# Performance work log

Hardware: AMD Instinct MI355X
Metric: run time of the kernel (lower is better)

The kernel has to match this reference:

```python
import jax, jax.numpy as jnp
import numpy as np

B, S, HID = 2, 2048, 4096
NH, NKV = 32, 8
HD = HID // NH          # 128
G = NH // NKV           # 4 groups per kv head
ROPE_THETA = 10000.0


def setup_inputs() -> dict:
    key = jax.random.key(0)
    ks = jax.random.split(key, 5)
    scale = 0.02
    return {
        "hidden_states": jax.random.normal(ks[0], (B, S, HID), dtype=jnp.float32),
        "Wq": jax.random.normal(ks[1], (NH * HD, HID), dtype=jnp.float32) * scale,
        "Wk": jax.random.normal(ks[2], (NKV * HD, HID), dtype=jnp.float32) * scale,
        "Wv": jax.random.normal(ks[3], (NKV * HD, HID), dtype=jnp.float32) * scale,
        "Wo": jax.random.normal(ks[4], (HID, HID), dtype=jnp.float32) * scale,
    }


def _rope_cos_sin(seq_len, head_dim, dtype):
    inv_freq = 1.0 / (ROPE_THETA ** (jnp.arange(0, head_dim, 2, dtype=jnp.float32) / head_dim))
    pos = jnp.arange(seq_len, dtype=jnp.float32)
    freqs = pos[:, None] * inv_freq[None, :]          # [S, HD/2]
    emb = jnp.concatenate([freqs, freqs], axis=-1)    # [S, HD]  (Llama: duplicated halves)
    return jnp.cos(emb).astype(dtype), jnp.sin(emb).astype(dtype)


def _rotate_half(x):
    x1, x2 = jnp.split(x, 2, axis=-1)
    return jnp.concatenate([-x2, x1], axis=-1)


def _apply_rope(x, cos, sin):
    # x: [B, H, S, HD]; cos/sin: [S, HD]
    return x * cos[None, None] + _rotate_half(x) * sin[None, None]


def reference(hidden_states, Wq, Wk, Wv, Wo):
    bsz, q_len, _ = hidden_states.shape
    dt = hidden_states.dtype

    q = (hidden_states @ Wq.T).reshape(bsz, q_len, NH, HD).transpose(0, 2, 1, 3)    # [B,NH,S,HD]
    k = (hidden_states @ Wk.T).reshape(bsz, q_len, NKV, HD).transpose(0, 2, 1, 3)   # [B,NKV,S,HD]
    v = (hidden_states @ Wv.T).reshape(bsz, q_len, NKV, HD).transpose(0, 2, 1, 3)   # [B,NKV,S,HD]

    cos, sin = _rope_cos_sin(q_len, HD, dt)
    q = _apply_rope(q, cos, sin)
    k = _apply_rope(k, cos, sin)

    # GQA: group queries per kv head instead of materializing repeat_kv
    qg = q.reshape(bsz, NKV, G, q_len, HD)                                          # [B,NKV,G,S,HD]
    scores = jnp.einsum("bkgqd,bkvd->bkgqv", qg, k) * (1.0 / np.sqrt(HD))           # [B,NKV,G,S,S]

    causal = jnp.tril(jnp.ones((q_len, q_len), dtype=bool))
    scores = jnp.where(causal[None, None, None], scores, jnp.finfo(jnp.float32).min)

    probs = jax.nn.softmax(scores.astype(jnp.float32), axis=-1).astype(dt)
    out = jnp.einsum("bkgqv,bkvd->bkgqd", probs, v)                                 # [B,NKV,G,S,HD]
    out = out.reshape(bsz, NH, q_len, HD).transpose(0, 2, 1, 3).reshape(bsz, q_len, HID)
    return out @ Wo.T
```

## Files before the change

### kernel.cpp

```cpp
#include <hip/hip_runtime.h>

typedef unsigned short u16;
typedef unsigned int u32;
typedef __attribute__((ext_vector_type(8))) short short8;
typedef __attribute__((ext_vector_type(4))) float f32x4;
typedef __attribute__((ext_vector_type(4))) u16 ushort4_t;

__device__ __forceinline__ float bf2f(u16 u) {
    u32 x = ((u32)u) << 16;
    return __uint_as_float(x);
}
__device__ __forceinline__ u16 f2bf(float f) {
    u32 x = __float_as_uint(f);
    x += 0x7FFFu + ((x >> 16) & 1u);
    return (u16)(x >> 16);
}
__device__ __forceinline__ u32 cvtpk_bf16(float lo, float hi) {
    u32 r;
    asm("v_cvt_pk_bf16_f32 %0, %1, %2" : "=v"(r) : "v"(lo), "v"(hi));
    return r;
}
__device__ __forceinline__ float exp2_hw(float x) {
    float r;
    asm("v_exp_f32 %0, %1" : "=v"(r) : "v"(x));
    return r;
}

using as1_cv = __attribute__((address_space(1))) const void;
using as3_v  = __attribute__((address_space(3))) void;
__device__ __forceinline__ void gld16(const void* g, void* l) {
    __builtin_amdgcn_global_load_lds((as1_cv*)g, (as3_v*)l, 16, 0, 0);
}

__global__ void cvt_f32_bf16(const float* __restrict__ in, u16* __restrict__ out, int n4) {
    int i = blockIdx.x * 256 + threadIdx.x;
    if (i >= n4) return;
    float4 v = ((const float4*)in)[i];
    ushort4_t o;
    o[0] = f2bf(v.x); o[1] = f2bf(v.y); o[2] = f2bf(v.z); o[3] = f2bf(v.w);
    ((ushort4_t*)out)[i] = o;
}

template <int OUT_MODE>
__global__ __launch_bounds__(256) void gemm_bt(
    const u16* __restrict__ A, const u16* __restrict__ B,
    u16* __restrict__ Cb, float* __restrict__ Cf,
    int M, int N, int K)
{
    __shared__ __align__(16) u16 As[128 * 32];
    __shared__ __align__(16) u16 Bs[128 * 32];
    const int t    = threadIdx.x;
    const int lane = t & 63;
    const int w    = t >> 6;
    const int wm   = w & 1;
    const int wn   = w >> 1;
    const int bx   = blockIdx.x;
    const int by   = blockIdx.y;

    const int r  = t >> 2;
    const int c8 = (t & 3) * 8;
    const u16* gA0 = A + (size_t)(by * 128 + r) * K + c8;
    const u16* gA1 = gA0 + (size_t)64 * K;
    const u16* gB0 = B + (size_t)(bx * 128 + r) * K + c8;
    const u16* gB1 = gB0 + (size_t)64 * K;
    u16* lA0 = &As[t * 8];
    u16* lA1 = &As[2048 + t * 8];
    u16* lB0 = &Bs[t * 8];
    u16* lB1 = &Bs[2048 + t * 8];

    f32x4 acc[4][4] = {};

    const int arow = wm * 64 + (lane & 15);
    const int brow = wn * 64 + (lane & 15);
    const int koff = (lane >> 4) * 8;

    for (int kt = 0; kt < K; kt += 32) {
        gld16(gA0 + kt, lA0);
        gld16(gA1 + kt, lA1);
        gld16(gB0 + kt, lB0);
        gld16(gB1 + kt, lB1);
        __syncthreads();
        short8 af[4], bf[4];
#pragma unroll
        for (int i = 0; i < 4; i++)
            af[i] = *(const short8*)&As[(arow + i * 16) * 32 + koff];
#pragma unroll
        for (int i = 0; i < 4; i++)
            bf[i] = *(const short8*)&Bs[(brow + i * 16) * 32 + koff];
#pragma unroll
        for (int mi = 0; mi < 4; mi++)
#pragma unroll
            for (int ni = 0; ni < 4; ni++)
                acc[mi][ni] = __builtin_amdgcn_mfma_f32_16x16x32_bf16(
                    af[mi], bf[ni], acc[mi][ni], 0, 0, 0);
        __syncthreads();
    }

    const int row0 = by * 128 + wm * 64 + (lane >> 4) * 4;
    const int col0 = bx * 128 + wn * 64 + (lane & 15);
#pragma unroll
    for (int mi = 0; mi < 4; mi++) {
#pragma unroll
        for (int ni = 0; ni < 4; ni++) {
            if (OUT_MODE == 3) {
                ushort4_t o;
#pragma unroll
                for (int rr = 0; rr < 4; rr++) o[rr] = f2bf(acc[mi][ni][rr]);
                int col = col0 + ni * 16;
                *(ushort4_t*)&Cb[(size_t)col * M + row0 + mi * 16] = o;
            } else {
#pragma unroll
                for (int rr = 0; rr < 4; rr++) {
                    int row = row0 + mi * 16 + rr;
                    int col = col0 + ni * 16;
                    float v = acc[mi][ni][rr];
                    if (OUT_MODE == 1) Cf[(size_t)row * N + col] = v;
                    else               Cb[(size_t)row * N + col] = f2bf(v);
                }
            }
        }
    }
}

template <int OUT_MODE>
__global__ __launch_bounds__(512, 2) void gemm_bt256(
    const u16* __restrict__ A, const u16* __restrict__ B,
    u16* __restrict__ Cb, float* __restrict__ Cf,
    int M, int N, int K)
{
    __shared__ __align__(16) u16 S[65536];
    const int t    = threadIdx.x;
    const int lane = t & 63;
    const int w    = t >> 6;
    const int wm   = w >> 2;
    const int wn   = w & 3;
    const int col  = lane & 15;
    const int g    = lane >> 4;

    const int kel = (((t & 3) ^ ((t >> 4) & 3)) * 8);
    const u16* gA = A + (size_t)(blockIdx.y * 256 + (t >> 2)) * K + kel;
    const u16* gB = B + (size_t)(blockIdx.x * 256 + (t >> 2)) * K + kel;
    const size_t rstride = (size_t)128 * K;
    u16* ldsA = &S[t * 8];
    u16* ldsB = &S[8192 + t * 8];

    const int rchunk = (((col * 4 + g) ^ ((col >> 2) & 3)) * 8);
    int aoff[8], boff[4];
#pragma unroll
    for (int mi = 0; mi < 8; mi++) aoff[mi] = (wm * 8 + mi) * 512 + rchunk;
#pragma unroll
    for (int ni = 0; ni < 4; ni++) boff[ni] = 8192 + (wn * 4 + ni) * 512 + rchunk;

    f32x4 acc[8][4] = {};

    auto STAGE = [&](int slot, int kt) {
        const size_t so = (size_t)slot * 16384;
        gld16(gA + kt,            ldsA + so);
        gld16(gA + kt + rstride,  ldsA + so + 4096);
        gld16(gB + kt,            ldsB + so);
        gld16(gB + kt + rstride,  ldsB + so + 4096);
    };

    const int NT = K >> 5;
    STAGE(0, 0);
    STAGE(1, 32);
    STAGE(2, 64);

    for (int kt = 0; kt < NT; kt++) {
        if (kt < NT - 2)      asm volatile("s_waitcnt vmcnt(8)" ::: "memory");
        else if (kt < NT - 1) asm volatile("s_waitcnt vmcnt(4)" ::: "memory");
        else                  asm volatile("s_waitcnt vmcnt(0)" ::: "memory");
        __builtin_amdgcn_s_barrier();
        asm volatile("" ::: "memory");
        if (kt < NT - 3) STAGE((kt + 3) & 3, (kt + 3) << 5);

        const u16* Sb = &S[(kt & 3) * 16384];
        short8 af[8], bf[4];
#pragma unroll
        for (int mi = 0; mi < 8; mi++) af[mi] = *(const short8*)(Sb + aoff[mi]);
#pragma unroll
        for (int ni = 0; ni < 4; ni++) bf[ni] = *(const short8*)(Sb + boff[ni]);

        __builtin_amdgcn_s_setprio(1);
#pragma unroll
        for (int mi = 0; mi < 8; mi++)
#pragma unroll
            for (int ni = 0; ni < 4; ni++)
                acc[mi][ni] = __builtin_amdgcn_mfma_f32_16x16x32_bf16(
                    af[mi], bf[ni], acc[mi][ni], 0, 0, 0);
        __builtin_amdgcn_s_setprio(0);
    }

    const int row0 = blockIdx.y * 256 + wm * 128 + (lane >> 4) * 4;
    const int col0 = blockIdx.x * 256 + wn * 64 + (lane & 15);
#pragma unroll
    for (int mi = 0; mi < 8; mi++) {
#pragma unroll
        for (int ni = 0; ni < 4; ni++) {
#pragma unroll
            for (int rr = 0; rr < 4; rr++) {
                int row = row0 + mi * 16 + rr;
                int col = col0 + ni * 16;
                float v = acc[mi][ni][rr];
                if (OUT_MODE == 1) Cf[(size_t)row * N + col] = v;
                else               Cb[(size_t)row * N + col] = f2bf(v);
            }
        }
    }
}

__global__ void rope_k(u16* __restrict__ x, int hshift) {
    int idx = blockIdx.x * 256 + threadIdx.x;
    int i   = idx & 63;
    int hm  = (1 << (hshift - 6)) - 1;
    int h   = (idx >> 6) & hm;
    int row = idx >> hshift;
    int s   = row & 2047;
    int stride = (hm + 1) * 128;
    size_t base = (size_t)row * stride + h * 128 + i;
    float th = (float)s * exp2f(-(float)i * 0.20762050593045952f);
    float cs = cosf(th), sn = sinf(th);
    float x1 = bf2f(x[base]), x2 = bf2f(x[base + 64]);
    x[base]      = f2bf(x1 * cs - x2 * sn);
    x[base + 64] = f2bf(x2 * cs + x1 * sn);
}

__global__ __launch_bounds__(256) void flash_attn(
    const u16* __restrict__ qb, const u16* __restrict__ kb,
    const u16* __restrict__ vt, u16* __restrict__ ob)
{
    __shared__ __align__(16) u16 Ks[2][64 * 128];
    __shared__ __align__(16) u16 Vs[2][128 * 64];
    const int t    = threadIdx.x;
    const int lane = t & 63;
    const int w    = t >> 6;
    const int col  = lane & 15;
    const int g    = lane >> 4;
    const int p    = blockIdx.x;
    const int qh   = blockIdx.y;
    const int b    = blockIdx.z;
    const int kvh  = qh >> 2;

    const u16* kbase = kb + ((size_t)b * 2048) * 1024 + kvh * 128;
    const u16* vbase = vt + ((size_t)kvh * 128) * 4096 + (size_t)b * 2048;

    const int ksw = ((t >> 4) & 3) ^ (((t >> 4) & 8) >> 1);
    const u16* ksrc0 = kbase + (size_t)(t >> 4) * 1024 + (size_t)((t & 15) ^ ksw) * 8;
    const u16* vsrc0 = vbase + (size_t)(t >> 3) * 4096 + (size_t)(((t & 7) ^ ((t >> 3) & 7)) * 8);
    u16* kdst = &Ks[0][0] + t * 8;
    u16* vdst = &Vs[0][0] + t * 8;

    const int swr = (col & 3) ^ (((col >> 2) & 1) << 2);
    int kb_[2][2];
#pragma unroll
    for (int h = 0; h < 2; h++)
#pragma unroll
        for (int kk = 0; kk < 2; kk++)
            kb_[h][kk] = (h * 32 + (col >> 2) * 8 + kk * 4 + (col & 3)) * 16;
    int cco[4];
#pragma unroll
    for (int c = 0; c < 4; c++) cco[c] = (c * 4 + g) ^ swr;
    const int vrow = col * 8;
    const int vcc0 = (g) ^ (col & 7);
    const int vcc1 = (4 + g) ^ (col & 7);

    const float SCL = 0.08838834764831845f * 1.4426950408889634f;

    auto STAGE = [&](int bufi, int k0i) {
#pragma unroll
        for (int i = 0; i < 4; i++)
            gld16(ksrc0 + (size_t)k0i * 1024 + (size_t)i * 16384, kdst + bufi * 8192 + i * 2048);
#pragma unroll
        for (int i = 0; i < 4; i++)
            gld16(vsrc0 + (size_t)i * 131072 + k0i, vdst + bufi * 8192 + i * 2048);
    };

#pragma unroll 1
    for (int phase = 0; phase < 2; phase++) {
        const int qt = phase ? (7 - p) : (8 + p);
        const int Q0 = qt * 128;
        const int qw = Q0 + w * 32;

        short8 qf[2][4];
#pragma unroll
        for (int sub = 0; sub < 2; sub++) {
            const u16* qrow = qb + ((size_t)(b * 2048 + qw + sub * 16 + col)) * 4096 + qh * 128;
#pragma unroll
            for (int c = 0; c < 4; c++)
                qf[sub][c] = *(const short8*)(qrow + c * 32 + g * 8);
        }

        float m_run[2] = {0.f, 0.f};
        float l_run[2] = {0.f, 0.f};
        f32x4 ot[2][8] = {};

        const int nsteps = (Q0 + 128) >> 6;
        const int qmax_w = qw + 31;

        int buf = 0;
        STAGE(0, 0);
        __syncthreads();

        for (int step = 0; step < nsteps; step++) {
            const int k0 = step << 6;
            if (step + 1 < nsteps) STAGE(buf ^ 1, k0 + 64);

            if (k0 <= qmax_w) {
                const u16* Kp = &Ks[buf][0];
                const u16* Vp = &Vs[buf][0];

                f32x4 sc[2][2][2] = {};
                __builtin_amdgcn_s_setprio(1);
#pragma unroll
                for (int h = 0; h < 2; h++)
#pragma unroll
                    for (int c = 0; c < 4; c++)
#pragma unroll
                        for (int kk = 0; kk < 2; kk++) {
                            short8 kf = *(const short8*)(Kp + (size_t)(kb_[h][kk] + cco[c]) * 8);
                            sc[0][h][kk] = __builtin_amdgcn_mfma_f32_16x16x32_bf16(kf, qf[0][c], sc[0][h][kk], 0, 0, 0);
                            sc[1][h][kk] = __builtin_amdgcn_mfma_f32_16x16x32_bf16(kf, qf[1][c], sc[1][h][kk], 0, 0, 0);
                        }
                __builtin_amdgcn_s_setprio(0);

                const bool full = (k0 + 63 <= qw);
                short8 pf[2][2];
#pragma unroll
                for (int sub = 0; sub < 2; sub++) {
                    float s[16];
                    float tmax = -1e30f;
                    if (full) {
#pragma unroll
                        for (int h = 0; h < 2; h++)
#pragma unroll
                            for (int kk = 0; kk < 2; kk++)
#pragma unroll
                                for (int rr = 0; rr < 4; rr++) {
                                    float v = sc[sub][h][kk][rr] * SCL;
                                    s[h * 8 + kk * 4 + rr] = v;
                                    tmax = fmaxf(tmax, v);
                                }
                    } else {
                        const int q = qw + sub * 16 + col;
#pragma unroll
                        for (int h = 0; h < 2; h++)
#pragma unroll
                            for (int kk = 0; kk < 2; kk++)
#pragma unroll
                                for (int rr = 0; rr < 4; rr++) {
                                    int key = k0 + h * 32 + g * 8 + kk * 4 + rr;
                                    float v = sc[sub][h][kk][rr] * SCL;
                                    v = (key <= q) ? v : -1e30f;
                                    s[h * 8 + kk * 4 + rr] = v;
                                    tmax = fmaxf(tmax, v);
                                }
                    }
                    tmax = fmaxf(tmax, __shfl_xor(tmax, 16));
                    tmax = fmaxf(tmax, __shfl_xor(tmax, 32));
                    if (__any(tmax > m_run[sub] + 8.0f)) {
                        float m_new = fmaxf(m_run[sub], tmax);
                        float alpha = exp2_hw(m_run[sub] - m_new);
                        l_run[sub] *= alpha;
                        m_run[sub] = m_new;
#pragma unroll
                        for (int dt = 0; dt < 8; dt++)
#pragma unroll
                            for (int rr = 0; rr < 4; rr++) ot[sub][dt][rr] *= alpha;
                    }
                    const float m = m_run[sub];
                    float tsum = 0.f;
#pragma unroll
                    for (int j = 0; j < 16; j++) {
                        s[j] = exp2_hw(s[j] - m);
                        tsum += s[j];
                    }
#pragma unroll
                    for (int h = 0; h < 2; h++)
#pragma unroll
                        for (int jw = 0; jw < 4; jw++)
                            ((u32*)&pf[sub][h])[jw] = cvtpk_bf16(s[h * 8 + jw * 2], s[h * 8 + jw * 2 + 1]);
                    tsum += __shfl_xor(tsum, 16);
                    tsum += __shfl_xor(tsum, 32);
                    l_run[sub] += tsum;
                }

                __builtin_amdgcn_s_setprio(1);
#pragma unroll
                for (int dt = 0; dt < 8; dt++) {
                    short8 vf0 = *(const short8*)(Vp + (size_t)(dt * 128 + vrow + vcc0) * 8);
                    short8 vf1 = *(const short8*)(Vp + (size_t)(dt * 128 + vrow + vcc1) * 8);
                    ot[0][dt] = __builtin_amdgcn_mfma_f32_16x16x32_bf16(vf0, pf[0][0], ot[0][dt], 0, 0, 0);
                    ot[1][dt] = __builtin_amdgcn_mfma_f32_16x16x32_bf16(vf0, pf[1][0], ot[1][dt], 0, 0, 0);
                    ot[0][dt] = __builtin_amdgcn_mfma_f32_16x16x32_bf16(vf1, pf[0][1], ot[0][dt], 0, 0, 0);
                    ot[1][dt] = __builtin_amdgcn_mfma_f32_16x16x32_bf16(vf1, pf[1][1], ot[1][dt], 0, 0, 0);
                }
                __builtin_amdgcn_s_setprio(0);
            }
            __syncthreads();
            buf ^= 1;
        }

#pragma unroll
        for (int sub = 0; sub < 2; sub++) {
            float inv = 1.0f / l_run[sub];
            u16* orow = ob + ((size_t)(b * 2048 + qw + sub * 16 + col)) * 4096 + qh * 128;
#pragma unroll
            for (int dt = 0; dt < 8; dt++) {
                ushort4_t o;
#pragma unroll
                for (int rr = 0; rr < 4; rr++) o[rr] = f2bf(ot[sub][dt][rr] * inv);
                *(ushort4_t*)(orow + dt * 16 + g * 4) = o;
            }
        }
    }
}

extern "C" void kernel_launch(void* const* d_in, const int* in_sizes, int n_in,
                              void* d_out, int out_size, void* d_ws, size_t ws_size,
                              hipStream_t stream) {
    const float* hs = (const float*)d_in[0];
    const float* Wq = (const float*)d_in[1];
    const float* Wk = (const float*)d_in[2];
    const float* Wv = (const float*)d_in[3];
    const float* Wo = (const float*)d_in[4];
    float* out = (float*)d_out;

    char* ws = (char*)d_ws;
    u16* hsb = (u16*)(ws + 0);
    u16* Wqb = (u16*)(ws + 33554432);
    u16* Wkb = (u16*)(ws + 67108864);
    u16* Wvb = (u16*)(ws + 75497472);
    u16* Wob = (u16*)(ws + 83886080);
    u16* qb  = (u16*)(ws + 117440512);
    u16* kbf = (u16*)(ws + 150994944);
    u16* vtb = (u16*)(ws + 159383552);
    u16* ab  = hsb;

    cvt_f32_bf16<<<16384, 256, 0, stream>>>(hs, hsb, 4194304);
    cvt_f32_bf16<<<16384, 256, 0, stream>>>(Wq, Wqb, 4194304);
    cvt_f32_bf16<<<4096,  256, 0, stream>>>(Wk, Wkb, 1048576);
    cvt_f32_bf16<<<4096,  256, 0, stream>>>(Wv, Wvb, 1048576);
    cvt_f32_bf16<<<16384, 256, 0, stream>>>(Wo, Wob, 4194304);

    gemm_bt256<0><<<dim3(16, 16), 512, 0, stream>>>(hsb, Wqb, qb,  nullptr, 4096, 4096, 4096);
    gemm_bt<0><<<dim3(8, 32),  256, 0, stream>>>(hsb, Wkb, kbf, nullptr, 4096, 1024, 4096);
    gemm_bt<3><<<dim3(8, 32),  256, 0, stream>>>(hsb, Wvb, vtb, nullptr, 4096, 1024, 4096);

    rope_k<<<32768, 256, 0, stream>>>(qb,  11);
    rope_k<<<8192,  256, 0, stream>>>(kbf, 9);

    flash_attn<<<dim3(8, 32, 2), 256, 0, stream>>>(qb, kbf, vtb, ab);

    gemm_bt256<1><<<dim3(16, 16), 512, 0, stream>>>(ab, Wob, nullptr, out, 4096, 4096, 4096);
}
```

Before: 845.5 us.

## Use 512-thread attention blocks with triple-buffered K/V and prescaled Q

```diff
diff --git a/kernel.cpp b/kernel.cpp
--- a/kernel.cpp
+++ b/kernel.cpp
@@ -209,7 +209,7 @@
     }
 }
 
-__global__ void rope_k(u16* __restrict__ x, int hshift) {
+__global__ void rope_k(u16* __restrict__ x, int hshift, float scale) {
     int idx = blockIdx.x * 256 + threadIdx.x;
     int i   = idx & 63;
     int hm  = (1 << (hshift - 6)) - 1;
@@ -221,16 +221,16 @@
     float th = (float)s * exp2f(-(float)i * 0.20762050593045952f);
     float cs = cosf(th), sn = sinf(th);
     float x1 = bf2f(x[base]), x2 = bf2f(x[base + 64]);
-    x[base]      = f2bf(x1 * cs - x2 * sn);
-    x[base + 64] = f2bf(x2 * cs + x1 * sn);
-}
-
-__global__ __launch_bounds__(256) void flash_attn(
+    x[base]      = f2bf((x1 * cs - x2 * sn) * scale);
+    x[base + 64] = f2bf((x2 * cs + x1 * sn) * scale);
+}
+
+__global__ __launch_bounds__(512) void flash_attn(
     const u16* __restrict__ qb, const u16* __restrict__ kb,
     const u16* __restrict__ vt, u16* __restrict__ ob)
 {
-    __shared__ __align__(16) u16 Ks[2][64 * 128];
-    __shared__ __align__(16) u16 Vs[2][128 * 64];
+    __shared__ __align__(16) u16 Ks[3][64 * 128];
+    __shared__ __align__(16) u16 Vs[3][128 * 64];
     const int t    = threadIdx.x;
     const int lane = t & 63;
     const int w    = t >> 6;
@@ -264,21 +264,18 @@
     const int vcc0 = (g) ^ (col & 7);
     const int vcc1 = (4 + g) ^ (col & 7);
 
-    const float SCL = 0.08838834764831845f * 1.4426950408889634f;
-
-    auto STAGE = [&](int bufi, int k0i) {
-#pragma unroll
-        for (int i = 0; i < 4; i++)
-            gld16(ksrc0 + (size_t)k0i * 1024 + (size_t)i * 16384, kdst + bufi * 8192 + i * 2048);
-#pragma unroll
-        for (int i = 0; i < 4; i++)
-            gld16(vsrc0 + (size_t)i * 131072 + k0i, vdst + bufi * 8192 + i * 2048);
+    auto STAGE = [&](int slot, int k0i) {
+        const size_t so = (size_t)slot * 8192;
+        gld16(ksrc0 + (size_t)k0i * 1024,        kdst + so);
+        gld16(ksrc0 + (size_t)(k0i + 32) * 1024, kdst + so + 4096);
+        gld16(vsrc0 + k0i,                       vdst + so);
+        gld16(vsrc0 + (size_t)64 * 4096 + k0i,   vdst + so + 4096);
     };
 
 #pragma unroll 1
     for (int phase = 0; phase < 2; phase++) {
-        const int qt = phase ? (7 - p) : (8 + p);
-        const int Q0 = qt * 128;
+        const int qt = phase ? (3 - p) : (4 + p);
+        const int Q0 = qt * 256;
         const int qw = Q0 + w * 32;
 
         short8 qf[2][4];
@@ -294,20 +291,27 @@
         float l_run[2] = {0.f, 0.f};
         f32x4 ot[2][8] = {};
 
-        const int nsteps = (Q0 + 128) >> 6;
+        const int nsteps = (Q0 + 256) >> 6;
         const int qmax_w = qw + 31;
 
-        int buf = 0;
         STAGE(0, 0);
-        __syncthreads();
+        STAGE(1, 64);
+        int slc = 0;
 
         for (int step = 0; step < nsteps; step++) {
             const int k0 = step << 6;
-            if (step + 1 < nsteps) STAGE(buf ^ 1, k0 + 64);
+            if (step + 1 < nsteps) asm volatile("s_waitcnt vmcnt(4)" ::: "memory");
+            else                   asm volatile("s_waitcnt vmcnt(0)" ::: "memory");
+            __builtin_amdgcn_s_barrier();
+            asm volatile("" ::: "memory");
+            if (step + 2 < nsteps) {
+                int sl2 = slc + 2; if (sl2 >= 3) sl2 -= 3;
+                STAGE(sl2, (step + 2) << 6);
+            }
 
             if (k0 <= qmax_w) {
-                const u16* Kp = &Ks[buf][0];
-                const u16* Vp = &Vs[buf][0];
+                const u16* Kp = &Ks[slc][0];
+                const u16* Vp = &Vs[slc][0];
 
                 f32x4 sc[2][2][2] = {};
                 __builtin_amdgcn_s_setprio(1);
@@ -336,7 +340,7 @@
                             for (int kk = 0; kk < 2; kk++)
 #pragma unroll
                                 for (int rr = 0; rr < 4; rr++) {
-                                    float v = sc[sub][h][kk][rr] * SCL;
+                                    float v = sc[sub][h][kk][rr];
                                     s[h * 8 + kk * 4 + rr] = v;
                                     tmax = fmaxf(tmax, v);
                                 }
@@ -349,7 +353,7 @@
 #pragma unroll
                                 for (int rr = 0; rr < 4; rr++) {
                                     int key = k0 + h * 32 + g * 8 + kk * 4 + rr;
-                                    float v = sc[sub][h][kk][rr] * SCL;
+                                    float v = sc[sub][h][kk][rr];
                                     v = (key <= q) ? v : -1e30f;
                                     s[h * 8 + kk * 4 + rr] = v;
                                     tmax = fmaxf(tmax, v);
@@ -396,9 +400,9 @@
                 }
                 __builtin_amdgcn_s_setprio(0);
             }
-            __syncthreads();
-            buf ^= 1;
+            slc = (slc == 2) ? 0 : slc + 1;
         }
+        __syncthreads();
 
 #pragma unroll
         for (int sub = 0; sub < 2; sub++) {
@@ -446,10 +450,10 @@
     gemm_bt<0><<<dim3(8, 32),  256, 0, stream>>>(hsb, Wkb, kbf, nullptr, 4096, 1024, 4096);
     gemm_bt<3><<<dim3(8, 32),  256, 0, stream>>>(hsb, Wvb, vtb, nullptr, 4096, 1024, 4096);
 
-    rope_k<<<32768, 256, 0, stream>>>(qb,  11);
-    rope_k<<<8192,  256, 0, stream>>>(kbf, 9);
-
-    flash_attn<<<dim3(8, 32, 2), 256, 0, stream>>>(qb, kbf, vtb, ab);
+    rope_k<<<32768, 256, 0, stream>>>(qb,  11, 0.08838834764831845f * 1.4426950408889634f);
+    rope_k<<<8192,  256, 0, stream>>>(kbf, 9, 1.0f);
+
+    flash_attn<<<dim3(4, 32, 2), 512, 0, stream>>>(qb, kbf, vtb, ab);
 
     gemm_bt256<1><<<dim3(16, 16), 512, 0, stream>>>(ab, Wob, nullptr, out, 4096, 4096, 4096);
 }
```

After: 782.4 us. 7.5% less time.
